# Kernel optimization log

Hardware: AMD Instinct MI355X
Metric: run time of the kernel (lower is better)

## Reference

```python
import jax, jax.numpy as jnp
import numpy as np


def _causal_conv(x, w, b, stride, dilation):
    # x: [N, Cin, T], w: [Cout, Cin, K] -> [N, Cout, L] (VALID, like the torch module which pads nothing)
    y = jax.lax.conv_general_dilated(
        x, w, window_strides=(stride,), padding='VALID',
        rhs_dilation=(dilation,), dimension_numbers=('NCH', 'OIH', 'NCH'))
    return y + b[None, :, None]


def setup_inputs() -> dict:
    key = jax.random.key(0)
    ks = jax.random.split(key, 7)
    B, S, F, T, Cin, Hid = 16, 64, 8, 512, 4, 16
    x = jax.random.normal(ks[0], (B, S, F, T, Cin), dtype=jnp.float32)
    w1 = jax.random.normal(ks[1], (Hid, Cin, 6), dtype=jnp.float32) * (1.0 / np.sqrt(Cin * 6))
    b1 = jax.random.normal(ks[2], (Hid,), dtype=jnp.float32) * 0.05
    w2 = jax.random.normal(ks[3], (Hid, Hid, 4), dtype=jnp.float32) * (1.0 / np.sqrt(Hid * 4))
    b2 = jax.random.normal(ks[4], (Hid,), dtype=jnp.float32) * 0.05
    w3 = jax.random.normal(ks[5], (Hid, Hid, 13), dtype=jnp.float32) * (1.0 / np.sqrt(Hid * 13))
    b3 = jax.random.normal(ks[6], (Hid,), dtype=jnp.float32) * 0.05
    return {"x": x, "w1": w1, "b1": b1, "w2": w2, "b2": b2, "w3": w3, "b3": b3, "etcn": 48}


def reference(x, w1, b1, w2, b2, w3, b3, etcn):
    # x: [B, S, F, T, Cin] -> fold station/filter dims into batch, one conv per stage
    B, S, F, T, Cin = x.shape
    xf = jnp.transpose(x, (0, 1, 2, 4, 3)).reshape(B * S * F, Cin, T)
    o1 = jax.nn.leaky_relu(_causal_conv(xf, w1, b1, stride=3, dilation=1))
    o2 = jax.nn.leaky_relu(_causal_conv(o1, w2, b2, stride=1, dilation=2))
    o3 = jax.nn.leaky_relu(_causal_conv(o2, w3, b3, stride=2, dilation=4))
    # truncate to expected_time_cell_num and stack the 3 scales: [N, 3, Hid, etcn]
    stk = jnp.stack([o1[:, :, :etcn], o2[:, :, :etcn], o3[:, :, :etcn]], axis=1)
    stk = jnp.transpose(stk, (0, 1, 3, 2))  # [N, 3, etcn, Hid]
    Hid = w1.shape[0]
    return stk.reshape(B, S, F, 3, etcn, Hid)
```

## Files before the change

### kernel.cpp

```cpp
#include <hip/hip_runtime.h>


typedef __attribute__((ext_vector_type(8))) short bf16x8;
typedef __attribute__((ext_vector_type(4))) float f32x4;
typedef __attribute__((ext_vector_type(4))) unsigned int u32x4;

union FragU { u32x4 u; bf16x8 b; };

__device__ __forceinline__ unsigned short f2bf(float f) {
    unsigned int u = __builtin_bit_cast(unsigned int, f);
    u += 0x7FFFu + ((u >> 16) & 1u);
    return (unsigned short)(u >> 16);
}
__device__ __forceinline__ unsigned int pack2bf(float lo, float hi) {
    return (unsigned int)f2bf(lo) | ((unsigned int)f2bf(hi) << 16);
}

__global__ void wtrans_kernel(const float* __restrict__ w1, const float* __restrict__ b1,
                              const float* __restrict__ w2, const float* __restrict__ b2,
                              const float* __restrict__ w3, const float* __restrict__ b3,
                              unsigned int* __restrict__ ws) {
    const int tid = threadIdx.x;
    if (tid < 256) {
        int kp = tid >> 4, co = tid & 15;
        int k0 = 2 * kp, k1 = k0 + 1;
        float v0 = (k0 < 24) ? w1[co * 24 + (k0 & 3) * 6 + (k0 >> 2)] : 0.f;
        float v1 = (k1 < 24) ? w1[co * 24 + (k1 & 3) * 6 + (k1 >> 2)] : 0.f;
        ws[tid] = pack2bf(v0, v1);
    }
    for (int p = tid; p < 512; p += 256) {
        int kp = p >> 4, co = p & 15;
        int k0 = 2 * kp, ci0 = k0 & 15, kk = k0 >> 4;
        ws[256 + p] = pack2bf(w2[co * 64 + ci0 * 4 + kk],
                              w2[co * 64 + (ci0 + 1) * 4 + kk]);
    }
    for (int p = tid; p < 1792; p += 256) {
        int kp = p >> 4, co = p & 15;
        int k0 = 2 * kp, ci0 = k0 & 15, kk = k0 >> 4;
        float v0 = (kk < 13) ? w3[co * 208 + ci0 * 13 + kk] : 0.f;
        float v1 = (kk < 13) ? w3[co * 208 + (ci0 + 1) * 13 + kk] : 0.f;
        ws[768 + p] = pack2bf(v0, v1);
    }
    float* wf = (float*)ws;
    if (tid < 16) { wf[2560 + tid] = b1[tid]; wf[2576 + tid] = b2[tid]; wf[2592 + tid] = b3[tid]; }
}

__global__ __launch_bounds__(64, 4) void itl_kernel(
    const float* __restrict__ x,
    const unsigned int* __restrict__ wt,
    float* __restrict__ out)
{
    __shared__ __align__(16) unsigned short o1b[160 * 24];
    __shared__ __align__(16) unsigned short o2e[76 * 24];

    const int lane = threadIdx.x;
    const int n    = blockIdx.x;
    const int co   = lane & 15;
    const int g    = lane >> 4;
    const int gh   = g >> 1;
    const int cib  = 8 * (g & 1);

    const float4* x4 = reinterpret_cast<const float4*>(x) + (size_t)n * 512;
    const float* wf  = (const float*)wt;
    float* outn = out + (size_t)n * 2304;

    if (lane < 48) ((unsigned int*)o2e)[72 * 12 + lane] = 0u;

    {
        FragU b1f;
        #pragma unroll
        for (int p = 0; p < 4; ++p) b1f.u[p] = wt[(4 * g + p) * 16 + co];
        const float bias1 = wf[2560 + co];
        #pragma unroll
        for (int ti = 0; ti < 10; ++ti) {
            const int j0 = 16 * ti;
            const int t  = j0 + co;
            float4 xa = x4[3 * t + 2 * g];
            float4 xb = x4[3 * t + 2 * g + 1];
            FragU a;
            a.u[0] = pack2bf(xa.x, xa.y);
            a.u[1] = pack2bf(xa.z, xa.w);
            a.u[2] = pack2bf(xb.x, xb.y);
            a.u[3] = pack2bf(xb.z, xb.w);
            f32x4 acc = {bias1, bias1, bias1, bias1};
            acc = __builtin_amdgcn_mfma_f32_16x16x32_bf16(a.b, b1f.b, acc, 0, 0, 0);
            const int tD = j0 + 4 * g;
            #pragma unroll
            for (int r = 0; r < 4; ++r) {
                float v = acc[r]; v = fmaxf(v, 0.01f * v);
                o1b[(tD + r) * 24 + co] = f2bf(v);
                if (ti < 3) outn[(tD + r) * 16 + co] = v;
            }
        }
    }
    __syncthreads();

    {
        FragU b2f[2];
        #pragma unroll
        for (int kb = 0; kb < 2; ++kb)
            #pragma unroll
            for (int p = 0; p < 4; ++p)
                b2f[kb].u[p] = wt[256 + (16 * kb + 4 * g + p) * 16 + co];
        const float bias2 = wf[2576 + co];
        #pragma unroll
        for (int ti = 0; ti < 9; ++ti) {
            const int j0 = 16 * ti;
            f32x4 acc = {bias2, bias2, bias2, bias2};
            #pragma unroll
            for (int kb = 0; kb < 2; ++kb) {
                const int row = j0 + co + 2 * (2 * kb + gh);
                FragU a; a.u = *(const u32x4*)&o1b[row * 24 + cib];
                acc = __builtin_amdgcn_mfma_f32_16x16x32_bf16(a.b, b2f[kb].b, acc, 0, 0, 0);
            }
            const int jD = j0 + 4 * g;
            #pragma unroll
            for (int r = 0; r < 4; ++r) {
                float v = acc[r]; v = fmaxf(v, 0.01f * v);
                if ((r & 1) == 0) o2e[((jD + r) >> 1) * 24 + co] = f2bf(v);
                if (ti < 3) outn[768 + (jD + r) * 16 + co] = v;
            }
        }
    }
    __syncthreads();

    {
        FragU b3f[7];
        #pragma unroll
        for (int kb = 0; kb < 7; ++kb)
            #pragma unroll
            for (int p = 0; p < 4; ++p)
                b3f[kb].u[p] = wt[768 + (16 * kb + 4 * g + p) * 16 + co];
        const float bias3 = wf[2592 + co];
        #pragma unroll
        for (int ti = 0; ti < 3; ++ti) {
            const int t0 = 16 * ti;
            f32x4 acc = {bias3, bias3, bias3, bias3};
            #pragma unroll
            for (int kb = 0; kb < 7; ++kb) {
                const int row = t0 + co + 2 * (2 * kb + gh);
                FragU a; a.u = *(const u32x4*)&o2e[row * 24 + cib];
                acc = __builtin_amdgcn_mfma_f32_16x16x32_bf16(a.b, b3f[kb].b, acc, 0, 0, 0);
            }
            const int tD = t0 + 4 * g;
            #pragma unroll
            for (int r = 0; r < 4; ++r) {
                float v = acc[r]; v = fmaxf(v, 0.01f * v);
                outn[1536 + (tD + r) * 16 + co] = v;
            }
        }
    }
}

extern "C" void kernel_launch(void* const* d_in, const int* in_sizes, int n_in,
                              void* d_out, int out_size, void* d_ws, size_t ws_size,
                              hipStream_t stream) {
    const float* x  = (const float*)d_in[0];
    const float* w1 = (const float*)d_in[1];
    const float* b1 = (const float*)d_in[2];
    const float* w2 = (const float*)d_in[3];
    const float* b2 = (const float*)d_in[4];
    const float* w3 = (const float*)d_in[5];
    const float* b3 = (const float*)d_in[6];
    float* out = (float*)d_out;
    unsigned int* ws = (unsigned int*)d_ws;

    wtrans_kernel<<<1, 256, 0, stream>>>(w1, b1, w2, b2, w3, b3, ws);
    itl_kernel<<<8192, 64, 0, stream>>>(x, ws, out);
}
```

Before: 34.16 us.

## Fold weight repacking into main kernel, drop syncthreads and padded x loads

Removes the separate weight-transform kernel launch; each block now gathers and packs conv weights to bf16 directly from the original fp32 tensors. The two __syncthreads barriers are dropped because the block is a single 64-lane wavefront. Lanes in group 3 now skip the x loads that only fed zero-weight K padding. This trades a launch and a dependency for redundant per-block strided weight gathers, repeated across all 8192 blocks.

```diff
diff --git a/kernel.cpp b/kernel.cpp
--- a/kernel.cpp
+++ b/kernel.cpp
@@ -16,38 +16,11 @@
     return (unsigned int)f2bf(lo) | ((unsigned int)f2bf(hi) << 16);
 }
 
-__global__ void wtrans_kernel(const float* __restrict__ w1, const float* __restrict__ b1,
-                              const float* __restrict__ w2, const float* __restrict__ b2,
-                              const float* __restrict__ w3, const float* __restrict__ b3,
-                              unsigned int* __restrict__ ws) {
-    const int tid = threadIdx.x;
-    if (tid < 256) {
-        int kp = tid >> 4, co = tid & 15;
-        int k0 = 2 * kp, k1 = k0 + 1;
-        float v0 = (k0 < 24) ? w1[co * 24 + (k0 & 3) * 6 + (k0 >> 2)] : 0.f;
-        float v1 = (k1 < 24) ? w1[co * 24 + (k1 & 3) * 6 + (k1 >> 2)] : 0.f;
-        ws[tid] = pack2bf(v0, v1);
-    }
-    for (int p = tid; p < 512; p += 256) {
-        int kp = p >> 4, co = p & 15;
-        int k0 = 2 * kp, ci0 = k0 & 15, kk = k0 >> 4;
-        ws[256 + p] = pack2bf(w2[co * 64 + ci0 * 4 + kk],
-                              w2[co * 64 + (ci0 + 1) * 4 + kk]);
-    }
-    for (int p = tid; p < 1792; p += 256) {
-        int kp = p >> 4, co = p & 15;
-        int k0 = 2 * kp, ci0 = k0 & 15, kk = k0 >> 4;
-        float v0 = (kk < 13) ? w3[co * 208 + ci0 * 13 + kk] : 0.f;
-        float v1 = (kk < 13) ? w3[co * 208 + (ci0 + 1) * 13 + kk] : 0.f;
-        ws[768 + p] = pack2bf(v0, v1);
-    }
-    float* wf = (float*)ws;
-    if (tid < 16) { wf[2560 + tid] = b1[tid]; wf[2576 + tid] = b2[tid]; wf[2592 + tid] = b3[tid]; }
-}
-
 __global__ __launch_bounds__(64, 4) void itl_kernel(
     const float* __restrict__ x,
-    const unsigned int* __restrict__ wt,
+    const float* __restrict__ w1, const float* __restrict__ b1,
+    const float* __restrict__ w2, const float* __restrict__ b2,
+    const float* __restrict__ w3, const float* __restrict__ b3,
     float* __restrict__ out)
 {
     __shared__ __align__(16) unsigned short o1b[160 * 24];
@@ -61,27 +34,36 @@
     const int cib  = 8 * (g & 1);
 
     const float4* x4 = reinterpret_cast<const float4*>(x) + (size_t)n * 512;
-    const float* wf  = (const float*)wt;
     float* outn = out + (size_t)n * 2304;
 
-    if (lane < 48) ((unsigned int*)o2e)[72 * 12 + lane] = 0u;
+    if (lane < 48) reinterpret_cast<unsigned int*>(o2e)[72 * 12 + lane] = 0u;
 
     {
         FragU b1f;
         #pragma unroll
-        for (int p = 0; p < 4; ++p) b1f.u[p] = wt[(4 * g + p) * 16 + co];
-        const float bias1 = wf[2560 + co];
+        for (int p = 0; p < 4; ++p) {
+            if (g < 3) {
+                const int k0 = 8 * g + 2 * p;
+                b1f.u[p] = pack2bf(w1[co * 24 + (k0 & 3) * 6 + (k0 >> 2)],
+                                   w1[co * 24 + ((k0 + 1) & 3) * 6 + ((k0 + 1) >> 2)]);
+            } else b1f.u[p] = 0u;
+        }
+        const float bias1 = b1[co];
         #pragma unroll
         for (int ti = 0; ti < 10; ++ti) {
             const int j0 = 16 * ti;
-            const int t  = j0 + co;
-            float4 xa = x4[3 * t + 2 * g];
-            float4 xb = x4[3 * t + 2 * g + 1];
             FragU a;
-            a.u[0] = pack2bf(xa.x, xa.y);
-            a.u[1] = pack2bf(xa.z, xa.w);
-            a.u[2] = pack2bf(xb.x, xb.y);
-            a.u[3] = pack2bf(xb.z, xb.w);
+            if (g < 3) {
+                const int t = j0 + co;
+                float4 xa = x4[3 * t + 2 * g];
+                float4 xb = x4[3 * t + 2 * g + 1];
+                a.u[0] = pack2bf(xa.x, xa.y);
+                a.u[1] = pack2bf(xa.z, xa.w);
+                a.u[2] = pack2bf(xb.x, xb.y);
+                a.u[3] = pack2bf(xb.z, xb.w);
+            } else {
+                a.u[0] = 0u; a.u[1] = 0u; a.u[2] = 0u; a.u[3] = 0u;
+            }
             f32x4 acc = {bias1, bias1, bias1, bias1};
             acc = __builtin_amdgcn_mfma_f32_16x16x32_bf16(a.b, b1f.b, acc, 0, 0, 0);
             const int tD = j0 + 4 * g;
@@ -93,16 +75,19 @@
             }
         }
     }
-    __syncthreads();
 
     {
         FragU b2f[2];
         #pragma unroll
         for (int kb = 0; kb < 2; ++kb)
             #pragma unroll
-            for (int p = 0; p < 4; ++p)
-                b2f[kb].u[p] = wt[256 + (16 * kb + 4 * g + p) * 16 + co];
-        const float bias2 = wf[2576 + co];
+            for (int p = 0; p < 4; ++p) {
+                const int k0 = 32 * kb + 8 * g + 2 * p;
+                const int ci0 = k0 & 15, kk = k0 >> 4;
+                b2f[kb].u[p] = pack2bf(w2[co * 64 + ci0 * 4 + kk],
+                                       w2[co * 64 + (ci0 + 1) * 4 + kk]);
+            }
+        const float bias2 = b2[co];
         #pragma unroll
         for (int ti = 0; ti < 9; ++ti) {
             const int j0 = 16 * ti;
@@ -122,16 +107,20 @@
             }
         }
     }
-    __syncthreads();
 
     {
         FragU b3f[7];
         #pragma unroll
         for (int kb = 0; kb < 7; ++kb)
             #pragma unroll
-            for (int p = 0; p < 4; ++p)
-                b3f[kb].u[p] = wt[768 + (16 * kb + 4 * g + p) * 16 + co];
-        const float bias3 = wf[2592 + co];
+            for (int p = 0; p < 4; ++p) {
+                const int k0 = 32 * kb + 8 * g + 2 * p;
+                const int ci0 = k0 & 15, kk = k0 >> 4;
+                b3f[kb].u[p] = (kk < 13) ? pack2bf(w3[co * 208 + ci0 * 13 + kk],
+                                                   w3[co * 208 + (ci0 + 1) * 13 + kk])
+                                         : 0u;
+            }
+        const float bias3 = b3[co];
         #pragma unroll
         for (int ti = 0; ti < 3; ++ti) {
             const int t0 = 16 * ti;
@@ -163,8 +152,6 @@
     const float* w3 = (const float*)d_in[5];
     const float* b3 = (const float*)d_in[6];
     float* out = (float*)d_out;
-    unsigned int* ws = (unsigned int*)d_ws;
 
-    wtrans_kernel<<<1, 256, 0, stream>>>(w1, b1, w2, b2, w3, b3, ws);
-    itl_kernel<<<8192, 64, 0, stream>>>(x, ws, out);
+    itl_kernel<<<8192, 64, 0, stream>>>(x, w1, b1, w2, b2, w3, b3, out);
 }
```

Result: slower. 94.05 us (+175.3%).

## Transpose MFMA operands for vectorized stores and drop redundant syncs

Applied to the files above, without the earlier changes.

Swaps the MFMA A/B operands in all three conv stages, so each lane's accumulator holds four consecutive output channels for a single time step. The LeakyReLU results can then be written as float4 global stores and packed 8-byte LDS stores instead of scalar ones. It also uses the hardware v_cvt_pk_bf16_f32 conversion and skips the x loads for the lane group whose weights are zero padding. It removes the __syncthreads calls, relying on the block being a single 64-lane wavefront. The weight-transform kernel now launches 64 blocks that all write the same workspace, which is redundant work.

```diff
diff --git a/kernel.cpp b/kernel.cpp
--- a/kernel.cpp
+++ b/kernel.cpp
@@ -4,6 +4,7 @@
 typedef __attribute__((ext_vector_type(8))) short bf16x8;
 typedef __attribute__((ext_vector_type(4))) float f32x4;
 typedef __attribute__((ext_vector_type(4))) unsigned int u32x4;
+typedef __attribute__((ext_vector_type(2))) unsigned int u32x2;
 
 union FragU { u32x4 u; bf16x8 b; };
 
@@ -14,6 +15,11 @@
 }
 __device__ __forceinline__ unsigned int pack2bf(float lo, float hi) {
     return (unsigned int)f2bf(lo) | ((unsigned int)f2bf(hi) << 16);
+}
+__device__ __forceinline__ unsigned int cvtpk(float lo, float hi) {
+    unsigned int r;
+    asm("v_cvt_pk_bf16_f32 %0, %1, %2" : "=v"(r) : "v"(lo), "v"(hi));
+    return r;
 }
 
 __global__ void wtrans_kernel(const float* __restrict__ w1, const float* __restrict__ b1,
@@ -55,99 +61,109 @@
 
     const int lane = threadIdx.x;
     const int n    = blockIdx.x;
-    const int co   = lane & 15;
+    const int tc   = lane & 15;
     const int g    = lane >> 4;
     const int gh   = g >> 1;
     const int cib  = 8 * (g & 1);
+    const int cob  = 4 * g;
 
     const float4* x4 = reinterpret_cast<const float4*>(x) + (size_t)n * 512;
     const float* wf  = (const float*)wt;
     float* outn = out + (size_t)n * 2304;
 
-    if (lane < 48) ((unsigned int*)o2e)[72 * 12 + lane] = 0u;
+    if (lane < 48) reinterpret_cast<unsigned int*>(o2e)[72 * 12 + lane] = 0u;
 
     {
-        FragU b1f;
+        FragU wA;
         #pragma unroll
-        for (int p = 0; p < 4; ++p) b1f.u[p] = wt[(4 * g + p) * 16 + co];
-        const float bias1 = wf[2560 + co];
+        for (int p = 0; p < 4; ++p) wA.u[p] = wt[(4 * g + p) * 16 + tc];
+        const float4 bs = *reinterpret_cast<const float4*>(&wf[2560 + cob]);
         #pragma unroll
         for (int ti = 0; ti < 10; ++ti) {
-            const int j0 = 16 * ti;
-            const int t  = j0 + co;
-            float4 xa = x4[3 * t + 2 * g];
-            float4 xb = x4[3 * t + 2 * g + 1];
-            FragU a;
-            a.u[0] = pack2bf(xa.x, xa.y);
-            a.u[1] = pack2bf(xa.z, xa.w);
-            a.u[2] = pack2bf(xb.x, xb.y);
-            a.u[3] = pack2bf(xb.z, xb.w);
-            f32x4 acc = {bias1, bias1, bias1, bias1};
-            acc = __builtin_amdgcn_mfma_f32_16x16x32_bf16(a.b, b1f.b, acc, 0, 0, 0);
-            const int tD = j0 + 4 * g;
-            #pragma unroll
-            for (int r = 0; r < 4; ++r) {
-                float v = acc[r]; v = fmaxf(v, 0.01f * v);
-                o1b[(tD + r) * 24 + co] = f2bf(v);
-                if (ti < 3) outn[(tD + r) * 16 + co] = v;
+            const int t = 16 * ti + tc;
+            FragU xB;
+            if (g < 3) {
+                float4 xa = x4[3 * t + 2 * g];
+                float4 xb = x4[3 * t + 2 * g + 1];
+                xB.u[0] = cvtpk(xa.x, xa.y);
+                xB.u[1] = cvtpk(xa.z, xa.w);
+                xB.u[2] = cvtpk(xb.x, xb.y);
+                xB.u[3] = cvtpk(xb.z, xb.w);
+            } else {
+                xB.u[0] = 0u; xB.u[1] = 0u; xB.u[2] = 0u; xB.u[3] = 0u;
+            }
+            f32x4 acc = {bs.x, bs.y, bs.z, bs.w};
+            acc = __builtin_amdgcn_mfma_f32_16x16x32_bf16(wA.b, xB.b, acc, 0, 0, 0);
+            const float v0 = fmaxf(acc[0], 0.01f * acc[0]);
+            const float v1 = fmaxf(acc[1], 0.01f * acc[1]);
+            const float v2 = fmaxf(acc[2], 0.01f * acc[2]);
+            const float v3 = fmaxf(acc[3], 0.01f * acc[3]);
+            u32x2 pk = {cvtpk(v0, v1), cvtpk(v2, v3)};
+            *reinterpret_cast<u32x2*>(&o1b[t * 24 + cob]) = pk;
+            if (ti < 3) {
+                f32x4 o = {v0, v1, v2, v3};
+                *reinterpret_cast<f32x4*>(&outn[t * 16 + cob]) = o;
             }
         }
     }
-    __syncthreads();
 
     {
-        FragU b2f[2];
+        FragU w2f[2];
         #pragma unroll
         for (int kb = 0; kb < 2; ++kb)
             #pragma unroll
             for (int p = 0; p < 4; ++p)
-                b2f[kb].u[p] = wt[256 + (16 * kb + 4 * g + p) * 16 + co];
-        const float bias2 = wf[2576 + co];
+                w2f[kb].u[p] = wt[256 + (16 * kb + 4 * g + p) * 16 + tc];
+        const float4 bs = *reinterpret_cast<const float4*>(&wf[2576 + cob]);
         #pragma unroll
         for (int ti = 0; ti < 9; ++ti) {
-            const int j0 = 16 * ti;
-            f32x4 acc = {bias2, bias2, bias2, bias2};
+            const int j = 16 * ti + tc;
+            f32x4 acc = {bs.x, bs.y, bs.z, bs.w};
             #pragma unroll
             for (int kb = 0; kb < 2; ++kb) {
-                const int row = j0 + co + 2 * (2 * kb + gh);
+                const int row = j + 2 * (2 * kb + gh);
                 FragU a; a.u = *(const u32x4*)&o1b[row * 24 + cib];
-                acc = __builtin_amdgcn_mfma_f32_16x16x32_bf16(a.b, b2f[kb].b, acc, 0, 0, 0);
+                acc = __builtin_amdgcn_mfma_f32_16x16x32_bf16(w2f[kb].b, a.b, acc, 0, 0, 0);
             }
-            const int jD = j0 + 4 * g;
-            #pragma unroll
-            for (int r = 0; r < 4; ++r) {
-                float v = acc[r]; v = fmaxf(v, 0.01f * v);
-                if ((r & 1) == 0) o2e[((jD + r) >> 1) * 24 + co] = f2bf(v);
-                if (ti < 3) outn[768 + (jD + r) * 16 + co] = v;
+            const float v0 = fmaxf(acc[0], 0.01f * acc[0]);
+            const float v1 = fmaxf(acc[1], 0.01f * acc[1]);
+            const float v2 = fmaxf(acc[2], 0.01f * acc[2]);
+            const float v3 = fmaxf(acc[3], 0.01f * acc[3]);
+            if ((tc & 1) == 0) {
+                u32x2 pk = {cvtpk(v0, v1), cvtpk(v2, v3)};
+                *reinterpret_cast<u32x2*>(&o2e[(j >> 1) * 24 + cob]) = pk;
+            }
+            if (ti < 3) {
+                f32x4 o = {v0, v1, v2, v3};
+                *reinterpret_cast<f32x4*>(&outn[768 + j * 16 + cob]) = o;
             }
         }
     }
-    __syncthreads();
 
     {
-        FragU b3f[7];
+        FragU w3f[7];
         #pragma unroll
         for (int kb = 0; kb < 7; ++kb)
             #pragma unroll
             for (int p = 0; p < 4; ++p)
-                b3f[kb].u[p] = wt[768 + (16 * kb + 4 * g + p) * 16 + co];
-        const float bias3 = wf[2592 + co];
+                w3f[kb].u[p] = wt[768 + (16 * kb + 4 * g + p) * 16 + tc];
+        const float4 bs = *reinterpret_cast<const float4*>(&wf[2592 + cob]);
         #pragma unroll
         for (int ti = 0; ti < 3; ++ti) {
-            const int t0 = 16 * ti;
-            f32x4 acc = {bias3, bias3, bias3, bias3};
+            const int t = 16 * ti + tc;
+            f32x4 acc = {bs.x, bs.y, bs.z, bs.w};
             #pragma unroll
             for (int kb = 0; kb < 7; ++kb) {
-                const int row = t0 + co + 2 * (2 * kb + gh);
+                const int row = t + 2 * (2 * kb + gh);
                 FragU a; a.u = *(const u32x4*)&o2e[row * 24 + cib];
-                acc = __builtin_amdgcn_mfma_f32_16x16x32_bf16(a.b, b3f[kb].b, acc, 0, 0, 0);
+                acc = __builtin_amdgcn_mfma_f32_16x16x32_bf16(w3f[kb].b, a.b, acc, 0, 0, 0);
             }
-            const int tD = t0 + 4 * g;
-            #pragma unroll
-            for (int r = 0; r < 4; ++r) {
-                float v = acc[r]; v = fmaxf(v, 0.01f * v);
-                outn[1536 + (tD + r) * 16 + co] = v;
-            }
+            const float v0 = fmaxf(acc[0], 0.01f * acc[0]);
+            const float v1 = fmaxf(acc[1], 0.01f * acc[1]);
+            const float v2 = fmaxf(acc[2], 0.01f * acc[2]);
+            const float v3 = fmaxf(acc[3], 0.01f * acc[3]);
+            f32x4 o = {v0, v1, v2, v3};
+            *reinterpret_cast<f32x4*>(&outn[1536 + t * 16 + cob]) = o;
         }
     }
 }
@@ -165,6 +181,6 @@
     float* out = (float*)d_out;
     unsigned int* ws = (unsigned int*)d_ws;
 
-    wtrans_kernel<<<1, 256, 0, stream>>>(w1, b1, w2, b2, w3, b3, ws);
+    wtrans_kernel<<<64, 256, 0, stream>>>(w1, b1, w2, b2, w3, b3, ws);
     itl_kernel<<<8192, 64, 0, stream>>>(x, ws, out);
 }
```

New measurement: 36.79 us. 1.08x slower.
